# Kernel tuning notes

Measured on AMD Instinct MI355X. Metric: run time of the kernel, lower is better.

The kernel has to match this reference:

```python
import jax, jax.numpy as jnp
import numpy as np
import math

VOCAB = 32000
D_MODEL = 512
N_LAYERS = 6
N_HEADS = 8
DIM_FF = 2048
B, L = 4, 2048
MAX_LEN = 5000
EPS = 1e-5


def _pos_encoding(max_len, d_model):
    pe = np.zeros((max_len, d_model), dtype=np.float32)
    pos = np.arange(max_len)[:, None].astype(np.float32)
    div = np.exp(np.arange(0, d_model, 2).astype(np.float32) * (-math.log(10000.0) / d_model))
    pe[:, 0::2] = np.sin(pos * div)
    pe[:, 1::2] = np.cos(pos * div)
    return jnp.asarray(pe)


def setup_inputs() -> dict:
    key = jax.random.key(0)
    ks = jax.random.split(key, 16)
    s = 0.02
    d, f, Ly = D_MODEL, DIM_FF, N_LAYERS
    inp = {
        "src": jax.random.randint(ks[0], (B, L), 0, VOCAB, dtype=jnp.int32),
        "embed": jax.random.normal(ks[1], (VOCAB, d), jnp.float32) * s,
        "pe": _pos_encoding(MAX_LEN, d),
        "Wq": jax.random.normal(ks[2], (Ly, d, d), jnp.float32) * s,
        "bq": jnp.zeros((Ly, d), jnp.float32),
        "Wk": jax.random.normal(ks[3], (Ly, d, d), jnp.float32) * s,
        "bk": jnp.zeros((Ly, d), jnp.float32),
        "Wv": jax.random.normal(ks[4], (Ly, d, d), jnp.float32) * s,
        "bv": jnp.zeros((Ly, d), jnp.float32),
        "Wo": jax.random.normal(ks[5], (Ly, d, d), jnp.float32) * s,
        "bo": jnp.zeros((Ly, d), jnp.float32),
        "W1": jax.random.normal(ks[6], (Ly, d, f), jnp.float32) * s,
        "b1": jnp.zeros((Ly, f), jnp.float32),
        "W2": jax.random.normal(ks[7], (Ly, f, d), jnp.float32) * s,
        "b2": jnp.zeros((Ly, d), jnp.float32),
        "g1": jnp.ones((Ly, d), jnp.float32),
        "be1": jnp.zeros((Ly, d), jnp.float32),
        "g2": jnp.ones((Ly, d), jnp.float32),
        "be2": jnp.zeros((Ly, d), jnp.float32),
    }
    return inp


def _layernorm(x, g, b):
    mu = jnp.mean(x, axis=-1, keepdims=True)
    var = jnp.mean((x - mu) ** 2, axis=-1, keepdims=True)
    return (x - mu) * jax.lax.rsqrt(var + EPS) * g + b


def _encoder(src, embed, pe, Wq, bq, Wk, bk, Wv, bv, Wo, bo, W1, b1, W2, b2, g1, be1, g2, be2):
    Bb, Ll = src.shape
    H = N_HEADS
    hd = D_MODEL // H
    x = embed[src] + pe[:Ll]  # [B, L, D]
    for i in range(Wq.shape[0]):
        # NOTE: faithful to the source: .view(B, H, L, hd) with NO transpose
        q = (x @ Wq[i] + bq[i]).reshape(Bb, H, Ll, hd)
        k = (x @ Wk[i] + bk[i]).reshape(Bb, H, Ll, hd)
        v = (x @ Wv[i] + bv[i]).reshape(Bb, H, Ll, hd)
        scores = jnp.einsum('bhqd,bhkd->bhqk', q, k) / math.sqrt(hd)
        w = jax.nn.softmax(scores, axis=-1)
        o = jnp.einsum('bhqk,bhkd->bhqd', w, v)
        o = o.transpose(0, 2, 1, 3).reshape(Bb, Ll, D_MODEL)
        o = o @ Wo[i] + bo[i]
        x = _layernorm(x + o, g1[i], be1[i])
        ff = jax.nn.relu(x @ W1[i] + b1[i]) @ W2[i] + b2[i]
        x = _layernorm(x + ff, g2[i], be2[i])
    return x


def reference(src, embed, pe, Wq, bq, Wk, bk, Wv, bv, Wo, bo, W1, b1, W2, b2, g1, be1, g2, be2):
    return _encoder(src, embed, pe, Wq, bq, Wk, bk, Wv, bv, Wo, bo, W1, b1, W2, b2, g1, be1, g2, be2)
```

## Files before the change

kernel.cpp:

```cpp
#include <hip/hip_runtime.h>
#include <hip/hip_bf16.h>

typedef unsigned short u16;
typedef __attribute__((ext_vector_type(8))) short bf16x8;
typedef __attribute__((ext_vector_type(2))) unsigned u32x2;
typedef __attribute__((ext_vector_type(4))) float f32x4;
typedef __attribute__((ext_vector_type(16))) float f32x16;

#define B_  4
#define L_  2048
#define D_  512
#define H_  8
#define HD_ 64
#define FF_ 2048
#define NL_ 6
#define M_  8192
#define MB_ 1048576ULL

#if __has_builtin(__builtin_amdgcn_exp2f)
#define EX2 __builtin_amdgcn_exp2f
#else
#define EX2 exp2f
#endif

__device__ __forceinline__ float b2f(u16 u) {
    unsigned v = ((unsigned)u) << 16;
    return __builtin_bit_cast(float, v);
}
__device__ __forceinline__ u16 f2b(float f) {
    unsigned u = __builtin_bit_cast(unsigned, f);
    unsigned r = u + 0x7FFFu + ((u >> 16) & 1u);
    return (u16)(r >> 16);
}
__device__ __forceinline__ unsigned pack2_bf16(float a, float b) {
    __hip_bfloat162 h = __float22bfloat162_rn(make_float2(a, b));
    unsigned u;
    __builtin_memcpy(&u, &h, 4);
    return u;
}
__device__ __forceinline__ float inp(const void* p, size_t i, int fp32) {
    return fp32 ? ((const float*)p)[i] : b2f(((const u16*)p)[i]);
}
__device__ __forceinline__ void gl2lds16(const void* g, void* l) {
    __builtin_amdgcn_global_load_lds(
        (const __attribute__((address_space(1))) void*)g,
        (__attribute__((address_space(3))) void*)l, 16, 0, 0);
}
__device__ __forceinline__ void bar_lds() {
    asm volatile("s_waitcnt lgkmcnt(0)" ::: "memory");
    __builtin_amdgcn_s_barrier();
}

__global__ void probe_k(const unsigned* __restrict__ g1, int* __restrict__ flag) {
    flag[0] = (g1[0] == 0x3F800000u) ? 1 : 0;
}

__global__ __launch_bounds__(256) void transpose_layer_k2(const void* __restrict__ Wq,
                                                          const void* __restrict__ Wk,
                                                          const void* __restrict__ Wv,
                                                          const void* __restrict__ Wo,
                                                          const void* __restrict__ W1,
                                                          const void* __restrict__ W2,
                                                          size_t wo, size_t wf,
                                                          u16* __restrict__ Wt,
                                                          const int* __restrict__ flag) {
    __shared__ u16 tile[32][33];
    int fp32 = flag[0];
    int bid = blockIdx.x;
    const void* in;
    size_t off;
    u16* out;
    int rows, cols, tx, ty;
    if (bid < 1024) {
        int which = bid >> 8;
        in = (which == 0) ? Wq : (which == 1) ? Wk : (which == 2) ? Wv : Wo;
        off = wo;
        out = Wt + (size_t)which * (512 * 512);
        rows = 512; cols = 512;
        int t = bid & 255; tx = t & 15; ty = t >> 4;
    } else if (bid < 2048) {
        in = W1; off = wf; out = Wt + 4 * (512 * 512);
        rows = 512; cols = 2048;
        int t = bid - 1024; tx = t & 63; ty = t >> 6;
    } else {
        in = W2; off = wf; out = Wt + 4 * (512 * 512) + 512 * 2048;
        rows = 2048; cols = 512;
        int t = bid - 2048; tx = t & 15; ty = t >> 4;
    }
    int c0 = tx * 32, r0 = ty * 32;
    int lx = threadIdx.x & 31, ly = threadIdx.x >> 5;
    #pragma unroll
    for (int i = ly; i < 32; i += 8)
        tile[i][lx] = f2b(inp(in, off + (size_t)(r0 + i) * cols + c0 + lx, fp32));
    __syncthreads();
    #pragma unroll
    for (int i = ly; i < 32; i += 8)
        out[(size_t)(c0 + i) * rows + r0 + lx] = tile[lx][i];
}

__global__ __launch_bounds__(256) void embed_k(const int* __restrict__ src,
                                               const void* __restrict__ embed,
                                               const void* __restrict__ pe,
                                               float* __restrict__ xf,
                                               u16* __restrict__ xb,
                                               const int* __restrict__ flag) {
    int fp32 = flag[0];
    int idx = blockIdx.x * 256 + threadIdx.x;
    int m = idx >> 9;
    int d = idx & 511;
    int tok = src[m];
    float v = inp(embed, (size_t)tok * D_ + d, fp32)
            + inp(pe, (size_t)(m & (L_ - 1)) * D_ + d, fp32);
    xf[idx] = v;
    xb[idx] = f2b(v);
}

template <int TM, int TN, int WM, int WN, int WRITE_BF16, int RELU>
__device__ __forceinline__ void gemm_core(const u16* __restrict__ A,
                                          const u16* __restrict__ Bt,
                                          int tnB, int tnC,
                                          const void* __restrict__ bias, size_t boff,
                                          float* __restrict__ Cf, u16* __restrict__ Cb,
                                          int N, int K, int kbeg, int kend,
                                          float cscale, int fp32, int use_bias) {
    constexpr int BK = 32;
    __shared__ u16 Asm[TM * BK];
    __shared__ u16 Bsm[TN * BK];
    int tm = blockIdx.y * TM;
    int tid = threadIdx.x;
    int wave = tid >> 6, lane = tid & 63, quad = lane >> 4, l16 = lane & 15;
    constexpr int NWN = TN / WN;
    int wm = (wave / NWN) * WM, wn = (wave % NWN) * WN;
    constexpr int FI = WM / 16, FJ = WN / 16;
    constexpr int CA = TM / 64;
    constexpr int CB = TN / 64;

    int arowl = (lane >> 2);
    int akc   = (lane & 3) * 8;

    f32x4 acc[FI][FJ];
    #pragma unroll
    for (int i = 0; i < FI; i++)
        #pragma unroll
        for (int j = 0; j < FJ; j++) { f32x4 z = {0.f, 0.f, 0.f, 0.f}; acc[i][j] = z; }

    for (int k0 = kbeg; k0 < kend; k0 += BK) {
        __syncthreads();
        #pragma unroll
        for (int c = 0; c < CA; c++) {
            int chunk = wave * CA + c;
            int row = chunk * 16 + arowl;
            gl2lds16(A + (size_t)(tm + row) * K + k0 + akc, &Asm[chunk * 16 * BK]);
        }
        #pragma unroll
        for (int c = 0; c < CB; c++) {
            int chunk = wave * CB + c;
            int row = chunk * 16 + arowl;
            gl2lds16(Bt + (size_t)(tnB + row) * K + k0 + akc, &Bsm[chunk * 16 * BK]);
        }
        __syncthreads();
        bf16x8 af[FI], bfr[FJ];
        #pragma unroll
        for (int i = 0; i < FI; i++)
            af[i] = *(bf16x8*)&Asm[(wm + i * 16 + l16) * BK + quad * 8];
        #pragma unroll
        for (int j = 0; j < FJ; j++)
            bfr[j] = *(bf16x8*)&Bsm[(wn + j * 16 + l16) * BK + quad * 8];
        #pragma unroll
        for (int i = 0; i < FI; i++)
            #pragma unroll
            for (int j = 0; j < FJ; j++)
                acc[i][j] = __builtin_amdgcn_mfma_f32_16x16x32_bf16(af[i], bfr[j], acc[i][j], 0, 0, 0);
    }

    #pragma unroll
    for (int i = 0; i < FI; i++) {
        int row = tm + wm + i * 16 + quad * 4;
        #pragma unroll
        for (int j = 0; j < FJ; j++) {
            int col = tnC + wn + j * 16 + l16;
            float bv = use_bias ? inp(bias, boff + col, fp32) : 0.f;
            #pragma unroll
            for (int r = 0; r < 4; r++) {
                float v = (acc[i][j][r] + bv) * cscale;
                if (RELU) v = v > 0.f ? v : 0.f;
                size_t idx = (size_t)(row + r) * N + col;
                if (WRITE_BF16) Cb[idx] = f2b(v);
                else            Cf[idx] = v;
            }
        }
    }
}

__global__ __launch_bounds__(256) void gemm_qkv(const u16* A, const u16* Wt,
                                                const void* bq, const void* bk, const void* bv,
                                                size_t boff, u16* Qb, u16* Kb, u16* Vb,
                                                int K, float qscale, const int* flag) {
    int tnB = blockIdx.x * 128;
    int mat = tnB >> 9;
    int tnC = tnB & 511;
    u16* Cb = (mat == 0) ? Qb : (mat == 1) ? Kb : Vb;
    const void* bias = (mat == 0) ? bq : (mat == 1) ? bk : bv;
    float sc = (mat == 0) ? qscale : 1.0f;
    gemm_core<128, 128, 64, 64, 1, 0>(A, Wt, tnB, tnC, bias, boff, nullptr, Cb, 512, K, 0, K, sc, flag[0], 1);
}
__global__ __launch_bounds__(256) void gemm128_b16_relu(const u16* A, const u16* Bt, const void* bias, size_t boff,
                                                        u16* Cb, int N, int K, const int* flag) {
    int tn = blockIdx.x * 128;
    gemm_core<128, 128, 64, 64, 1, 1>(A, Bt, tn, tn, bias, boff, nullptr, Cb, N, K, 0, K, 1.0f, flag[0], 1);
}
__global__ __launch_bounds__(256) void gemm64_f32_sk(const u16* A, const u16* Bt, const void* bias, size_t boff,
                                                     float* Cf, int N, int K, const int* flag) {
    int tn = blockIdx.x * 128;
    int z = blockIdx.z;
    int ks = K / gridDim.z;
    gemm_core<64, 128, 64, 32, 0, 0>(A, Bt, tn, tn, bias, boff, Cf + (size_t)z * M_ * 512, nullptr,
                                     N, K, z * ks, z * ks + ks, 1.0f, flag[0], z == 0);
}

__global__ __launch_bounds__(256) void vperm_k(const u16* __restrict__ in, u16* __restrict__ out) {
    __shared__ u16 tile[32][33];
    int bh = blockIdx.z;
    const u16* pin = in + (size_t)bh * (L_ * HD_);
    u16* pout = out + (size_t)bh * (L_ * HD_);
    int c0 = blockIdx.x * 32, r0 = blockIdx.y * 32;
    int lx = threadIdx.x & 31, ly = threadIdx.x >> 5;
    #pragma unroll
    for (int i = ly; i < 32; i += 8)
        tile[i][lx] = pin[(size_t)(r0 + i) * HD_ + c0 + lx];
    __syncthreads();
    #pragma unroll
    for (int i = ly; i < 32; i += 8)
        pout[(size_t)(c0 + i) * L_ + r0 + lx] = tile[lx][i];
}

__global__ __launch_bounds__(256) void attn_k(const u16* __restrict__ Q,
                                              const u16* __restrict__ K,
                                              const u16* __restrict__ Vt,
                                              u16* __restrict__ O) {
    constexpr int LD = 72;
    constexpr int NT = L_ / 64;
    __shared__ u16 Ks[64 * LD];
    __shared__ u16 Vs[64 * LD];
    __shared__ u16 Ps[64 * LD];
    __shared__ float Ls[64];
    int qt = blockIdx.x;
    int bh = blockIdx.y;
    int b = bh >> 3, h = bh & 7;
    size_t hb = (size_t)bh * (L_ * HD_);
    int tid = threadIdx.x;
    int wave = tid >> 6, lane = tid & 63, hi = lane >> 5, r32 = lane & 31;
    int wq = wave >> 1, wc = wave & 1;

    int srow[2], scol[2];
    #pragma unroll
    for (int s = 0; s < 2; s++) { int v = tid + s * 256; srow[s] = v >> 3; scol[s] = (v & 7) * 8; }

    bf16x8 kreg[2], vreg[2];
    #pragma unroll
    for (int s = 0; s < 2; s++) {
        kreg[s] = *(const bf16x8*)(K + hb + (size_t)srow[s] * HD_ + scol[s]);
        vreg[s] = *(const bf16x8*)(Vt + hb + (size_t)srow[s] * L_ + scol[s]);
    }

    #pragma unroll
    for (int s = 0; s < 2; s++)
        *(bf16x8*)&Ps[srow[s] * LD + scol[s]] =
            *(const bf16x8*)(Q + hb + (size_t)(qt * 64 + srow[s]) * HD_ + scol[s]);
    bar_lds();
    bf16x8 aq[4];
    #pragma unroll
    for (int dc = 0; dc < 4; dc++)
        aq[dc] = *(bf16x8*)&Ps[(wq * 32 + r32) * LD + dc * 16 + hi * 8];
    bar_lds();

    bf16x8 vones;
    #pragma unroll
    for (int i = 0; i < 8; i++) vones[i] = (short)0x3F80;

    f32x16 oac, lac;
    #pragma unroll
    for (int i = 0; i < 16; i++) { oac[i] = 0.f; lac[i] = 0.f; }

    for (int kt = 0; kt < NT; kt++) {
        #pragma unroll
        for (int s = 0; s < 2; s++) {
            *(bf16x8*)&Ks[srow[s] * LD + scol[s]] = kreg[s];
            *(bf16x8*)&Vs[srow[s] * LD + scol[s]] = vreg[s];
        }
        bar_lds();
        if (kt + 1 < NT) {
            #pragma unroll
            for (int s = 0; s < 2; s++) {
                kreg[s] = *(const bf16x8*)(K + hb + (size_t)((kt + 1) * 64 + srow[s]) * HD_ + scol[s]);
                vreg[s] = *(const bf16x8*)(Vt + hb + (size_t)srow[s] * L_ + (kt + 1) * 64 + scol[s]);
            }
        }

        f32x16 sac;
        #pragma unroll
        for (int i = 0; i < 16; i++) sac[i] = 0.f;
        __builtin_amdgcn_s_setprio(1);
        #pragma unroll
        for (int dc = 0; dc < 4; dc++) {
            bf16x8 bk = *(bf16x8*)&Ks[(wc * 32 + r32) * LD + dc * 16 + hi * 8];
            sac = __builtin_amdgcn_mfma_f32_32x32x16_bf16(aq[dc], bk, sac, 0, 0, 0);
        }
        __builtin_amdgcn_s_setprio(0);

        int pbase = (wq * 32 + 4 * hi) * LD + wc * 32 + r32;
        #pragma unroll
        for (int r = 0; r < 16; r++) {
            float p = EX2(sac[r]);
            Ps[pbase + ((r & 3) + 8 * (r >> 2)) * LD] = f2b(p);
        }
        bar_lds();

        __builtin_amdgcn_s_setprio(1);
        #pragma unroll
        for (int kc = 0; kc < 4; kc++) {
            bf16x8 ap = *(bf16x8*)&Ps[(wq * 32 + r32) * LD + kc * 16 + hi * 8];
            bf16x8 bv = *(bf16x8*)&Vs[(wc * 32 + r32) * LD + kc * 16 + hi * 8];
            oac = __builtin_amdgcn_mfma_f32_32x32x16_bf16(ap, bv, oac, 0, 0, 0);
            if (wc == 0)
                lac = __builtin_amdgcn_mfma_f32_32x32x16_bf16(ap, vones, lac, 0, 0, 0);
        }
        __builtin_amdgcn_s_setprio(0);
        bar_lds();
    }

    if (wc == 0 && r32 == 0) {
        #pragma unroll
        for (int r = 0; r < 16; r++)
            Ls[wq * 32 + 4 * hi + (r & 3) + 8 * (r >> 2)] = lac[r];
    }
    bar_lds();

    #pragma unroll
    for (int r = 0; r < 16; r++) {
        int row = wq * 32 + 4 * hi + (r & 3) + 8 * (r >> 2);
        float v = oac[r] * (1.0f / fmaxf(Ls[row], 1e-30f));
        int l2 = qt * 64 + row;
        O[((size_t)b * L_ + l2) * D_ + h * HD_ + wc * 32 + r32] = f2b(v);
    }
}

__global__ __launch_bounds__(256) void ln_k2(const float* resid,
                                             const float* __restrict__ delta0,
                                             const float* __restrict__ delta1,
                                             const void* __restrict__ g,
                                             const void* __restrict__ be, size_t goff,
                                             float* xf_out,
                                             void* __restrict__ out_raw,
                                             const int* __restrict__ flag,
                                             int two, int is_final) {
    int fp32 = flag[0];
    int row = blockIdx.x * 4 + (threadIdx.x >> 6);
    int lane = threadIdx.x & 63;
    const float* pr = resid + (size_t)row * D_;
    const float* pd0 = delta0 + (size_t)row * D_;
    const float* pd1 = delta1 + (size_t)row * D_;
    float u[8];
    float s = 0.f;
    #pragma unroll
    for (int i = 0; i < 8; i++) {
        int c = lane + i * 64;
        u[i] = pr[c] + pd0[c] + (two ? pd1[c] : 0.f);
        s += u[i];
    }
    #pragma unroll
    for (int d = 1; d < 64; d <<= 1) s += __shfl_xor(s, d);
    float mu = s * (1.0f / 512.0f);
    float vs = 0.f;
    #pragma unroll
    for (int i = 0; i < 8; i++) { float t = u[i] - mu; vs += t * t; }
    #pragma unroll
    for (int d = 1; d < 64; d <<= 1) vs += __shfl_xor(vs, d);
    float rstd = rsqrtf(vs * (1.0f / 512.0f) + 1e-5f);
    #pragma unroll
    for (int i = 0; i < 8; i++) {
        int c = lane + i * 64;
        float v = (u[i] - mu) * rstd * inp(g, goff + c, fp32) + inp(be, goff + c, fp32);
        xf_out[(size_t)row * D_ + c] = v;
        size_t oi = (size_t)row * D_ + c;
        if (is_final && fp32) ((float*)out_raw)[oi] = v;
        else                  ((u16*)out_raw)[oi]  = f2b(v);
    }
}

extern "C" void kernel_launch(void* const* d_in, const int* in_sizes, int n_in,
                              void* d_out, int out_size, void* d_ws, size_t ws_size,
                              hipStream_t stream) {
    (void)in_sizes; (void)n_in; (void)out_size;
    const int*  src   = (const int*)d_in[0];
    const void* embed = d_in[1];
    const void* pe    = d_in[2];
    const void* Wq = d_in[3];  const void* bq = d_in[4];
    const void* Wk = d_in[5];  const void* bk = d_in[6];
    const void* Wv = d_in[7];  const void* bv = d_in[8];
    const void* Wo = d_in[9];  const void* bo = d_in[10];
    const void* W1 = d_in[11]; const void* b1 = d_in[12];
    const void* W2 = d_in[13]; const void* b2 = d_in[14];
    const void* g1 = d_in[15]; const void* be1 = d_in[16];
    const void* g2 = d_in[17]; const void* be2 = d_in[18];

    int big = (ws_size >= 103 * MB_ + 64);
    char* ws = (char*)d_ws;
    float* xf  = (float*)(ws);
    u16*  xb   = (u16*)(ws + 16 * MB_);
    u16*  Qb   = (u16*)(ws + 24 * MB_);
    u16*  Kb   = (u16*)(ws + 32 * MB_);
    u16*  Vb   = (u16*)(ws + 40 * MB_);
    u16*  Vt   = (u16*)(ws + 48 * MB_);
    u16*  Ab   = (u16*)(ws + 56 * MB_);
    float* Pf0 = (float*)(ws + 24 * MB_);
    float* Pf1 = (float*)(ws + 40 * MB_);
    u16*  Hb   = (u16*)(ws + (big ? 64 : 40) * MB_);
    u16*  Wt   = (u16*)(ws + (big ? 96 : 72) * MB_);
    int*  flag = (int*)(ws + (big ? 102 : 78) * MB_);
    u16* Wot = Wt + 786432;
    u16* W1t = Wt + 1048576;
    u16* W2t = Wt + 2097152;

    const float QSCALE = 0.125f * 1.44269504f;

    probe_k<<<1, 1, 0, stream>>>((const unsigned*)g1, flag);
    embed_k<<<(M_ * D_) / 256, 256, 0, stream>>>(src, embed, pe, xf, xb, flag);

    for (int i = 0; i < NL_; i++) {
        size_t wo = (size_t)i * 512 * 512;
        size_t wf = (size_t)i * 512 * 2048;
        size_t vo = (size_t)i * 512;
        size_t fo = (size_t)i * 2048;
        transpose_layer_k2<<<3072, 256, 0, stream>>>(Wq, Wk, Wv, Wo, W1, W2, wo, wf, Wt, flag);

        gemm_qkv<<<dim3(12, 64), 256, 0, stream>>>(xb, Wt, bq, bk, bv, vo, Qb, Kb, Vb, 512, QSCALE, flag);
        vperm_k<<<dim3(2, 64, 32), 256, 0, stream>>>(Vb, Vt);
        attn_k<<<dim3(32, 32), 256, 0, stream>>>(Qb, Kb, Vt, Ab);
        gemm64_f32_sk<<<dim3(4, 128, 2), 256, 0, stream>>>(Ab, Wot, bo, vo, Pf0, 512, 512, flag);
        ln_k2<<<M_ / 4, 256, 0, stream>>>(xf, Pf0, Pf1, g1, be1, vo, xf, xb, flag, 1, 0);
        gemm128_b16_relu<<<dim3(16, 64), 256, 0, stream>>>(xb, W1t, b1, fo, Hb, 2048, 512, flag);
        if (big) gemm64_f32_sk<<<dim3(4, 128, 2), 256, 0, stream>>>(Hb, W2t, b2, vo, Pf0, 512, 2048, flag);
        else     gemm64_f32_sk<<<dim3(4, 128, 1), 256, 0, stream>>>(Hb, W2t, b2, vo, Pf0, 512, 2048, flag);
        void* out_raw = (i == NL_ - 1) ? d_out : (void*)xb;
        ln_k2<<<M_ / 4, 256, 0, stream>>>(xf, Pf0, Pf1, g2, be2, vo, xf, out_raw, flag, big ? 1 : 0, (i == NL_ - 1) ? 1 : 0);
    }
}
```

Baseline: 1.520 ms.

## Restructure attention to keep K/V/P in registers with split-K waves

The attention kernel stops staging K, V and P through LDS. Each wave now loads its own K and V fragments straight from global memory into registers and computes S transposed (K×Q), so the exp'd probabilities can be repacked in registers with permlane32 swaps and fed directly to the PV MFMA. The two waves per query tile split the key range and are combined in LDS at the end. The per-row softmax denominator is now summed in registers instead of via an extra MFMA against a ones vector. This removes all per-iteration barriers and LDS traffic, at the cost of redundant global loads of K/V across query-tile waves and a final cross-wave reduction.

```diff
diff --git a/kernel.cpp b/kernel.cpp
--- a/kernel.cpp
+++ b/kernel.cpp
@@ -45,10 +45,6 @@
     __builtin_amdgcn_global_load_lds(
         (const __attribute__((address_space(1))) void*)g,
         (__attribute__((address_space(3))) void*)l, 16, 0, 0);
-}
-__device__ __forceinline__ void bar_lds() {
-    asm volatile("s_waitcnt lgkmcnt(0)" ::: "memory");
-    __builtin_amdgcn_s_barrier();
 }
 
 __global__ void probe_k(const unsigned* __restrict__ g1, int* __restrict__ flag) {
@@ -234,114 +230,136 @@
         pout[(size_t)(c0 + i) * L_ + r0 + lx] = tile[lx][i];
 }
 
+__device__ __forceinline__ bf16x8 frag_from4(unsigned w0, unsigned w1, unsigned w2, unsigned w3) {
+    union { unsigned u[4]; bf16x8 v; } t;
+    t.u[0] = w0; t.u[1] = w1; t.u[2] = w2; t.u[3] = w3;
+    return t.v;
+}
+__device__ __forceinline__ void lane32_swap(unsigned& x, unsigned& y, int hi) {
+#if __has_builtin(__builtin_amdgcn_permlane32_swap)
+    u32x2 r = __builtin_amdgcn_permlane32_swap(x, y, false, false);
+    x = r[0]; y = r[1];
+#else
+    unsigned tx = (unsigned)__shfl_xor((int)x, 32, 64);
+    unsigned ty = (unsigned)__shfl_xor((int)y, 32, 64);
+    x = hi ? ty : x;
+    y = hi ? y : tx;
+#endif
+}
+
 __global__ __launch_bounds__(256) void attn_k(const u16* __restrict__ Q,
                                               const u16* __restrict__ K,
                                               const u16* __restrict__ Vt,
                                               u16* __restrict__ O) {
-    constexpr int LD = 72;
     constexpr int NT = L_ / 64;
-    __shared__ u16 Ks[64 * LD];
-    __shared__ u16 Vs[64 * LD];
-    __shared__ u16 Ps[64 * LD];
-    __shared__ float Ls[64];
+    __shared__ float Red[2][64][32];
+    __shared__ float LsP[2][2][2][32];
     int qt = blockIdx.x;
     int bh = blockIdx.y;
     int b = bh >> 3, h = bh & 7;
     size_t hb = (size_t)bh * (L_ * HD_);
-    int tid = threadIdx.x;
-    int wave = tid >> 6, lane = tid & 63, hi = lane >> 5, r32 = lane & 31;
-    int wq = wave >> 1, wc = wave & 1;
-
-    int srow[2], scol[2];
-    #pragma unroll
-    for (int s = 0; s < 2; s++) { int v = tid + s * 256; srow[s] = v >> 3; scol[s] = (v & 7) * 8; }
-
-    bf16x8 kreg[2], vreg[2];
-    #pragma unroll
-    for (int s = 0; s < 2; s++) {
-        kreg[s] = *(const bf16x8*)(K + hb + (size_t)srow[s] * HD_ + scol[s]);
-        vreg[s] = *(const bf16x8*)(Vt + hb + (size_t)srow[s] * L_ + scol[s]);
-    }
-
-    #pragma unroll
-    for (int s = 0; s < 2; s++)
-        *(bf16x8*)&Ps[srow[s] * LD + scol[s]] =
-            *(const bf16x8*)(Q + hb + (size_t)(qt * 64 + srow[s]) * HD_ + scol[s]);
-    bar_lds();
-    bf16x8 aq[4];
-    #pragma unroll
-    for (int dc = 0; dc < 4; dc++)
-        aq[dc] = *(bf16x8*)&Ps[(wq * 32 + r32) * LD + dc * 16 + hi * 8];
-    bar_lds();
-
-    bf16x8 vones;
-    #pragma unroll
-    for (int i = 0; i < 8; i++) vones[i] = (short)0x3F80;
-
-    f32x16 oac, lac;
-    #pragma unroll
-    for (int i = 0; i < 16; i++) { oac[i] = 0.f; lac[i] = 0.f; }
+    int tid = threadIdx.x, wave = tid >> 6, lane = tid & 63, hi = lane >> 5, r32 = lane & 31;
+    int wqq = wave >> 1, wk = wave & 1;
+
+    const u16* qp = Q + hb + (size_t)(qt * 64 + wqq * 32 + r32) * HD_ + hi * 8;
+    bf16x8 qf[4];
+    #pragma unroll
+    for (int dc = 0; dc < 4; dc++) qf[dc] = *(const bf16x8*)(qp + dc * 16);
+
+    const u16* kp = K + hb + (size_t)(wk * 32 + r32) * HD_ + hi * 8;
+    const u16* vp0 = Vt + hb + (size_t)r32 * L_ + wk * 32 + hi * 8;
+    const u16* vp1 = vp0 + (size_t)32 * L_;
+
+    bf16x8 kf[4], vf[4];
+    #pragma unroll
+    for (int dc = 0; dc < 4; dc++) kf[dc] = *(const bf16x8*)(kp + dc * 16);
+    vf[0] = *(const bf16x8*)(vp0);
+    vf[1] = *(const bf16x8*)(vp0 + 16);
+    vf[2] = *(const bf16x8*)(vp1);
+    vf[3] = *(const bf16x8*)(vp1 + 16);
+    kp += 64 * HD_; vp0 += 64; vp1 += 64;
+
+    f32x16 oac0, oac1;
+    #pragma unroll
+    for (int i = 0; i < 16; i++) { oac0[i] = 0.f; oac1[i] = 0.f; }
+    float ls = 0.f;
 
     for (int kt = 0; kt < NT; kt++) {
-        #pragma unroll
-        for (int s = 0; s < 2; s++) {
-            *(bf16x8*)&Ks[srow[s] * LD + scol[s]] = kreg[s];
-            *(bf16x8*)&Vs[srow[s] * LD + scol[s]] = vreg[s];
-        }
-        bar_lds();
+        f32x16 sac;
+        #pragma unroll
+        for (int i = 0; i < 16; i++) sac[i] = 0.f;
+        __builtin_amdgcn_s_setprio(1);
+        #pragma unroll
+        for (int dc = 0; dc < 4; dc++)
+            sac = __builtin_amdgcn_mfma_f32_32x32x16_bf16(kf[dc], qf[dc], sac, 0, 0, 0);
+        __builtin_amdgcn_s_setprio(0);
         if (kt + 1 < NT) {
             #pragma unroll
-            for (int s = 0; s < 2; s++) {
-                kreg[s] = *(const bf16x8*)(K + hb + (size_t)((kt + 1) * 64 + srow[s]) * HD_ + scol[s]);
-                vreg[s] = *(const bf16x8*)(Vt + hb + (size_t)srow[s] * L_ + (kt + 1) * 64 + scol[s]);
-            }
-        }
-
-        f32x16 sac;
-        #pragma unroll
-        for (int i = 0; i < 16; i++) sac[i] = 0.f;
+            for (int dc = 0; dc < 4; dc++) kf[dc] = *(const bf16x8*)(kp + dc * 16);
+            kp += 64 * HD_;
+        }
+
+        float p[16];
+        #pragma unroll
+        for (int r = 0; r < 16; r++) p[r] = EX2(sac[r]);
+        {
+            float a = (p[0] + p[1]) + (p[2] + p[3]);
+            float c = (p[4] + p[5]) + (p[6] + p[7]);
+            float e = (p[8] + p[9]) + (p[10] + p[11]);
+            float g = (p[12] + p[13]) + (p[14] + p[15]);
+            ls += (a + c) + (e + g);
+        }
+        bf16x8 pa[2];
+        #pragma unroll
+        for (int c = 0; c < 2; c++) {
+            int rb = c * 8;
+            unsigned a0 = pack2_bf16(p[rb + 0], p[rb + 1]);
+            unsigned a1 = pack2_bf16(p[rb + 2], p[rb + 3]);
+            unsigned a2 = pack2_bf16(p[rb + 4], p[rb + 5]);
+            unsigned a3 = pack2_bf16(p[rb + 6], p[rb + 7]);
+            lane32_swap(a0, a2, hi);
+            lane32_swap(a1, a3, hi);
+            pa[c] = frag_from4(a0, a1, a2, a3);
+        }
+
         __builtin_amdgcn_s_setprio(1);
-        #pragma unroll
-        for (int dc = 0; dc < 4; dc++) {
-            bf16x8 bk = *(bf16x8*)&Ks[(wc * 32 + r32) * LD + dc * 16 + hi * 8];
-            sac = __builtin_amdgcn_mfma_f32_32x32x16_bf16(aq[dc], bk, sac, 0, 0, 0);
-        }
+        oac0 = __builtin_amdgcn_mfma_f32_32x32x16_bf16(pa[0], vf[0], oac0, 0, 0, 0);
+        oac1 = __builtin_amdgcn_mfma_f32_32x32x16_bf16(pa[0], vf[2], oac1, 0, 0, 0);
+        oac0 = __builtin_amdgcn_mfma_f32_32x32x16_bf16(pa[1], vf[1], oac0, 0, 0, 0);
+        oac1 = __builtin_amdgcn_mfma_f32_32x32x16_bf16(pa[1], vf[3], oac1, 0, 0, 0);
         __builtin_amdgcn_s_setprio(0);
-
-        int pbase = (wq * 32 + 4 * hi) * LD + wc * 32 + r32;
+        if (kt + 1 < NT) {
+            vf[0] = *(const bf16x8*)(vp0);
+            vf[1] = *(const bf16x8*)(vp0 + 16);
+            vf[2] = *(const bf16x8*)(vp1);
+            vf[3] = *(const bf16x8*)(vp1 + 16);
+            vp0 += 64; vp1 += 64;
+        }
+    }
+
+    LsP[wqq][wk][hi][r32] = ls;
+    if (wk == 1) {
         #pragma unroll
         for (int r = 0; r < 16; r++) {
-            float p = EX2(sac[r]);
-            Ps[pbase + ((r & 3) + 8 * (r >> 2)) * LD] = f2b(p);
-        }
-        bar_lds();
-
-        __builtin_amdgcn_s_setprio(1);
-        #pragma unroll
-        for (int kc = 0; kc < 4; kc++) {
-            bf16x8 ap = *(bf16x8*)&Ps[(wq * 32 + r32) * LD + kc * 16 + hi * 8];
-            bf16x8 bv = *(bf16x8*)&Vs[(wc * 32 + r32) * LD + kc * 16 + hi * 8];
-            oac = __builtin_amdgcn_mfma_f32_32x32x16_bf16(ap, bv, oac, 0, 0, 0);
-            if (wc == 0)
-                lac = __builtin_amdgcn_mfma_f32_32x32x16_bf16(ap, vones, lac, 0, 0, 0);
-        }
-        __builtin_amdgcn_s_setprio(0);
-        bar_lds();
-    }
-
-    if (wc == 0 && r32 == 0) {
-        #pragma unroll
-        for (int r = 0; r < 16; r++)
-            Ls[wq * 32 + 4 * hi + (r & 3) + 8 * (r >> 2)] = lac[r];
-    }
-    bar_lds();
-
-    #pragma unroll
-    for (int r = 0; r < 16; r++) {
-        int row = wq * 32 + 4 * hi + (r & 3) + 8 * (r >> 2);
-        float v = oac[r] * (1.0f / fmaxf(Ls[row], 1e-30f));
-        int l2 = qt * 64 + row;
-        O[((size_t)b * L_ + l2) * D_ + h * HD_ + wc * 32 + r32] = f2b(v);
+            Red[wqq][lane][r]      = oac0[r];
+            Red[wqq][lane][16 + r] = oac1[r];
+        }
+    }
+    __syncthreads();
+    if (wk == 0) {
+        #pragma unroll
+        for (int r = 0; r < 16; r++) {
+            int qr = (r & 3) + 8 * (r >> 2) + 4 * hi;
+            float den = LsP[wqq][0][0][qr] + LsP[wqq][0][1][qr]
+                      + LsP[wqq][1][0][qr] + LsP[wqq][1][1][qr];
+            float inv = 1.0f / fmaxf(den, 1e-30f);
+            float v0 = (oac0[r] + Red[wqq][lane][r]) * inv;
+            float v1 = (oac1[r] + Red[wqq][lane][16 + r]) * inv;
+            int qg = qt * 64 + wqq * 32 + qr;
+            size_t ob = ((size_t)b * L_ + qg) * D_ + h * HD_;
+            O[ob + r32]      = f2b(v0);
+            O[ob + 32 + r32] = f2b(v1);
+        }
     }
 }
 
```

New measurement: 1.775 ms. 1.17x slower.
